# Optimization experiments

Measured on AMD Instinct MI355X. Metric: run time of the kernel, lower is better.

## Reference

```python
import jax, jax.numpy as jnp
import numpy as np

NUM_HEADS = 12
DIM_HEAD = 64
HIDDEN = 768


def _get_rel_pos(size, rel_pos):
    # q_size == k_size: relative coords in [0, 2*size-2]
    idx = jnp.arange(size)[:, None] - jnp.arange(size)[None, :] + (size - 1)
    return rel_pos[idx]  # (size, size, dim_head)


def setup_inputs() -> dict:
    key = jax.random.key(0)
    ks = jax.random.split(key, 5)
    B, H, W, C = 4, 32, 32, HIDDEN
    x = jax.random.normal(ks[0], (B, H, W, C), dtype=jnp.float32)
    w_qkv = jax.random.normal(ks[1], (C, 3 * NUM_HEADS * DIM_HEAD), dtype=jnp.float32) * (C ** -0.5)
    w_out = jax.random.normal(ks[2], (NUM_HEADS * DIM_HEAD, C), dtype=jnp.float32) * ((NUM_HEADS * DIM_HEAD) ** -0.5)
    b_out = jnp.zeros((C,), dtype=jnp.float32)
    rel_pos_h = jax.random.normal(ks[3], (2 * H - 1, DIM_HEAD), dtype=jnp.float32) * 0.02
    rel_pos_w = jax.random.normal(ks[4], (2 * W - 1, DIM_HEAD), dtype=jnp.float32) * 0.02
    return {"x": x, "w_qkv": w_qkv, "w_out": w_out, "b_out": b_out,
            "rel_pos_h": rel_pos_h, "rel_pos_w": rel_pos_w}


def reference(x, w_qkv, w_out, b_out, rel_pos_h, rel_pos_w):
    B, H, W, C = x.shape
    N = H * W
    nh, dh = NUM_HEADS, DIM_HEAD
    # qkv projection: (B, N, 3*nh*dh) split as (qkv, head, dim)
    qkv = x.reshape(B, N, C) @ w_qkv
    qkv = qkv.reshape(B, N, 3, nh, dh).transpose(2, 0, 3, 1, 4)  # (3, B, nh, N, dh)
    q, k, v = qkv[0], qkv[1], qkv[2]
    scale = dh ** -0.5
    attn = jnp.einsum('bhnd,bhmd->bhnm', q, k) * scale  # (B, nh, N, N)
    # decomposed relative positional bias (heads folded into batch)
    Rh = _get_rel_pos(H, rel_pos_h)  # (H, H, dh)
    Rw = _get_rel_pos(W, rel_pos_w)  # (W, W, dh)
    r_q = q.reshape(B * nh, H, W, dh)
    rel_h = jnp.einsum('bhwc,hkc->bhwk', r_q, Rh)  # (B*nh, H, W, H)
    rel_w = jnp.einsum('bhwc,wkc->bhwk', r_q, Rw)  # (B*nh, H, W, W)
    attn = (attn.reshape(B * nh, H, W, H, W)
            + rel_h[:, :, :, :, None]
            + rel_w[:, :, :, None, :]).reshape(B, nh, N, N)
    attn = jax.nn.softmax(attn, axis=-1)
    out = jnp.einsum('bhnm,bhmd->bhnd', attn, v)  # (B, nh, N, dh)
    out = out.transpose(0, 2, 1, 3).reshape(B, N, nh * dh)
    return out @ w_out + b_out  # (B, N, hidden)
```

## Files before the change

### kernel.cpp

```cpp
#include <hip/hip_runtime.h>
#include <cstdint>

#define DEV __device__ __forceinline__

typedef __bf16  bf16x8 __attribute__((ext_vector_type(8)));
typedef short   s16x8  __attribute__((ext_vector_type(8)));
typedef float   f32x4  __attribute__((ext_vector_type(4)));

#define QSCALE 0.18033688011112042f
#define MOFF   17.312340490667560f

DEV unsigned short f2bf(float f){
  union { float f; unsigned u; } v; v.f = f;
  unsigned r = v.u + 0x7fffu + ((v.u >> 16) & 1u);
  return (unsigned short)(r >> 16);
}

DEV unsigned pk2(float lo, float hi){
  unsigned a = __builtin_bit_cast(unsigned, lo) + 0x8000u;
  unsigned b = __builtin_bit_cast(unsigned, hi) + 0x8000u;
  return __builtin_amdgcn_perm(b, a, 0x07060302);
}

DEV void gl2lds16(const void* g, void* l){
  __builtin_amdgcn_global_load_lds((__attribute__((address_space(1))) void*)(void*)(g),
                                   (__attribute__((address_space(3))) void*)(l), 16, 0, 0);
}

DEV f32x4 mfma16(bf16x8 a, bf16x8 b, f32x4 c){
  return __builtin_amdgcn_mfma_f32_16x16x32_bf16(a, b, c, 0, 0, 0);
}

__global__ __launch_bounds__(256) void prep_kernel(const float* __restrict__ x,
                                                   short* __restrict__ xb,
                                                   const float* __restrict__ rph,
                                                   const float* __restrict__ rpw,
                                                   short* __restrict__ rphb,
                                                   short* __restrict__ rpwb,
                                                   const float* __restrict__ w_qkv,
                                                   short* __restrict__ wqT,
                                                   const float* __restrict__ w_out,
                                                   short* __restrict__ woT){
  __shared__ float tb[32][33];
  int b = blockIdx.x;
  if (b < 1536){
    int i = b * 256 + threadIdx.x;
    const float4* in4 = (const float4*)x;
    float4 f0 = in4[i*2], f1 = in4[i*2+1];
    s16x8 o;
    o[0]=(short)f2bf(f0.x); o[1]=(short)f2bf(f0.y); o[2]=(short)f2bf(f0.z); o[3]=(short)f2bf(f0.w);
    o[4]=(short)f2bf(f1.x); o[5]=(short)f2bf(f1.y); o[6]=(short)f2bf(f1.z); o[7]=(short)f2bf(f1.w);
    *(s16x8*)(xb + i*8) = o;
  } else if (b == 1536){
    int t = threadIdx.x;
    for (int j = 0; j < 16; j++){
      int idx = t*16 + j;
      if (idx < 4032){
        rphb[idx] = (short)f2bf(rph[idx] * 8.f);
        rpwb[idx] = (short)f2bf(rpw[idx] * 8.f);
      } else if (idx < 4096){
        rpwb[idx] = 0;
      }
    }
  } else {
    const float* in; short* out; int R, C, bx, by;
    if (b < 3265){ int t = b - 1537; in = w_qkv; out = wqT; R = 768; C = 2304; bx = t % 72; by = t / 72; }
    else         { int t = b - 3265; in = w_out; out = woT; R = 768; C = 768;  bx = t % 24; by = t / 24; }
    int tx = threadIdx.x & 31, ty = threadIdx.x >> 5;
    int c0 = bx * 32, r0 = by * 32;
    for (int i = 0; i < 4; i++)
      tb[ty + i*8][tx] = in[(r0 + ty + i*8)*C + c0 + tx];
    __syncthreads();
    for (int i = 0; i < 4; i++)
      out[(c0 + ty + i*8)*R + r0 + tx] = (short)f2bf(tb[tx][ty + i*8]);
  }
}

__global__ __launch_bounds__(256) void qkv_gemm_kernel(const short* __restrict__ xb,
                                                       const short* __restrict__ wqT,
                                                       short* __restrict__ qb,
                                                       short* __restrict__ kb,
                                                       short* __restrict__ vtb){
  __shared__ __align__(16) short As[128*64];
  __shared__ __align__(16) short Bs[96*64];
  const int tid = threadIdx.x, lane = tid & 63, wv = tid >> 6;
  const int quad = lane >> 4, mi = lane & 15;
  const int flat = blockIdx.x + (blockIdx.y << 5);
  const int xcd = flat & 7, s = flat >> 3;
  const int bx = (xcd & 3)*8 + (s & 7);
  const int by = (xcd >> 2)*12 + (s >> 3);
  const int m0 = bx * 128, n0 = by * 96;
  const int wrow = wv >> 1, wcol = wv & 1;
  const int srow = lane >> 3, scs = lane & 7;
  const int sc = scs ^ (srow & 7);
  f32x4 acc[4][3] = {};
  for (int k0 = 0; k0 < 768; k0 += 64){
    __syncthreads();
    for (int i = 0; i < 4; i++){
      int rbase = i*32 + wv*8;
      int row = rbase + srow;
      gl2lds16(xb + (m0+row)*768 + k0 + sc*8, As + rbase*64 + lane*8);
    }
    for (int i = 0; i < 3; i++){
      int rbase = i*32 + wv*8;
      int row = rbase + srow;
      gl2lds16(wqT + (n0+row)*768 + k0 + sc*8, Bs + rbase*64 + lane*8);
    }
    __syncthreads();
    bf16x8 a[2][4], b[2][3];
#pragma unroll
    for (int kk = 0; kk < 2; kk++){
      int ccs = ((quad + kk*4) ^ (mi & 7)) * 8;
      for (int mt = 0; mt < 4; mt++) a[kk][mt] = *(const bf16x8*)(As + (wrow*64 + mt*16 + mi)*64 + ccs);
      for (int nt = 0; nt < 3; nt++) b[kk][nt] = *(const bf16x8*)(Bs + (wcol*48 + nt*16 + mi)*64 + ccs);
    }
#pragma unroll
    for (int kk = 0; kk < 2; kk++)
      for (int mt = 0; mt < 4; mt++)
        for (int nt = 0; nt < 3; nt++)
          acc[mt][nt] = mfma16(a[kk][mt], b[kk][nt], acc[mt][nt]);
  }
  const int which = n0 / 768;
  if (which == 2){
    for (int nt = 0; nt < 3; nt++){
      int j = n0 + wcol*48 + nt*16 + mi;
      int rem = j % 768;
      int head = rem >> 6, d = rem & 63;
      for (int mt = 0; mt < 4; mt++)
        for (int r = 0; r < 4; r++){
          int m = m0 + wrow*64 + mt*16 + quad*4 + r;
          int bh = (m >> 10)*12 + head;
          vtb[((bh*64 + d) << 10) + (m & 1023)] = (short)f2bf(acc[mt][nt][r]);
        }
    }
  } else {
    const float qs = (which == 0) ? QSCALE : 1.0f;
    short* dst = (which == 0) ? qb : kb;
    for (int nt = 0; nt < 3; nt++){
      int j = n0 + wcol*48 + nt*16 + mi;
      int rem = j % 768;
      int head = rem >> 6, d = rem & 63;
      for (int mt = 0; mt < 4; mt++)
        for (int r = 0; r < 4; r++){
          int m = m0 + wrow*64 + mt*16 + quad*4 + r;
          int bh = (m >> 10)*12 + head;
          dst[((bh << 10) + (m & 1023))*64 + d] = (short)f2bf(acc[mt][nt][r] * qs);
        }
    }
  }
}

__global__ __launch_bounds__(256, 3) void flash_kernel(const short* __restrict__ qb,
                                                       const short* __restrict__ kb,
                                                       const short* __restrict__ vtb,
                                                       const short* __restrict__ rphb,
                                                       const short* __restrict__ rpwb,
                                                       short* __restrict__ ao){
  __shared__ __align__(16) char QE[16384];
  __shared__ __align__(16) short Kt[64*64];
  __shared__ __align__(16) short Vt[64*64];
  __shared__ __align__(16) short Pt[64*64];
  __shared__ __align__(16) float rHs[32*64];
  short* Qt = (short*)QE;
  float* Es = (float*)QE;
  const int tid = threadIdx.x, lane = tid & 63, wv = tid >> 6;
  const int quad = lane >> 4, mi = lane & 15;
  const int flat = blockIdx.x + (blockIdx.y << 4);
  const int nw = (flat & 7)*96 + (flat >> 3);
  const int bh = nw >> 4, n0 = (nw & 15) << 6;
  const int sw0 = (quad ^ (mi & 7)) * 8;
  const int sw1 = ((quad + 4) ^ (mi & 7)) * 8;
  const int qrow = wv*16 + mi;
  const int srow = lane >> 3;

  const short* kg = kb  + bh*1024*64;
  const short* vg = vtb + bh*64*1024;

  {
    const short* qg = qb + (bh*1024 + n0)*64;
    for (int i = 0; i < 2; i++){
      int slab = wv*2 + i, rbase = slab*8;
      int row = rbase + srow;
      int c = (lane & 7) ^ (row & 7);
      gl2lds16(qg + row*64 + c*8, Qt + rbase*64 + lane*8);
    }
  }
  __syncthreads();

  bf16x8 qf0 = *(const bf16x8*)(Qt + qrow*64 + sw0);
  bf16x8 qf1 = *(const bf16x8*)(Qt + qrow*64 + sw1);

  {
    int h = (n0 + wv*16) >> 5;
    const short* rp = rphb + (h + 31 - mi)*64;
#pragma unroll
    for (int khb = 0; khb < 2; khb++){
      const short* rk = rp - khb*1024;
      bf16x8 a0 = *(const bf16x8*)(rk + quad*8);
      bf16x8 a1 = *(const bf16x8*)(rk + 32 + quad*8);
      f32x4 c = {};
      c = mfma16(a0, qf0, c);
      c = mfma16(a1, qf1, c);
      for (int r = 0; r < 4; r++)
        rHs[(khb*16 + quad*4 + r)*64 + wv*16 + mi] = c[r] - MOFF;
    }
  }

  __syncthreads();

#pragma unroll
  for (int jt = 0; jt < 4; jt++){
    const short* rr = rpwb + (jt*16 + mi)*64;
    bf16x8 a0 = *(const bf16x8*)(rr + quad*8);
    bf16x8 a1 = *(const bf16x8*)(rr + 32 + quad*8);
    f32x4 c = {};
    c = mfma16(a0, qf0, c);
    c = mfma16(a1, qf1, c);
    for (int r = 0; r < 4; r++)
      Es[(jt*16 + quad*4 + r)*64 + qrow] = c[r];
  }
  float rw[2][4];
  {
    int w31 = (qrow & 31) + 31;
#pragma unroll
    for (int s = 0; s < 2; s++)
      for (int r = 0; r < 4; r++)
        rw[s][r] = Es[(w31 - (s*16 + quad*4 + r))*64 + qrow];
  }

  f32x4 O[4] = {};
  float l_ = 0.f;

  for (int step = 0; step < 16; step++){
    {
      const short* kt = kg + step*64*64;
      for (int i = 0; i < 2; i++){
        int slab = wv*2 + i, rbase = slab*8;
        int row = rbase + srow;
        int c = (lane & 7) ^ (row & 7);
        gl2lds16(kt + row*64 + c*8, Kt + rbase*64 + lane*8);
        gl2lds16(vg + row*1024 + step*64 + c*8, Vt + rbase*64 + lane*8);
      }
    }
    __syncthreads();

    f32x4 S[4];
#pragma unroll
    for (int nt = 0; nt < 4; nt++){
      bf16x8 kf0 = *(const bf16x8*)(Kt + (nt*16 + mi)*64 + sw0);
      bf16x8 kf1 = *(const bf16x8*)(Kt + (nt*16 + mi)*64 + sw1);
      f32x4 c = {};
      c = mfma16(kf0, qf0, c);
      c = mfma16(kf1, qf1, c);
      S[nt] = c;
    }
    float kh0 = rHs[(2*step)*64 + qrow];
    float kh1 = rHs[(2*step + 1)*64 + qrow];
#pragma unroll
    for (int nt = 0; nt < 4; nt++){
      float kh = (nt & 2) ? kh1 : kh0;
      for (int r = 0; r < 4; r++){
        float p = __builtin_amdgcn_exp2f(S[nt][r] + kh + rw[nt & 1][r]);
        S[nt][r] = p;
        l_ += p;
      }
    }
#pragma unroll
    for (int nt = 0; nt < 4; nt++){
      unsigned u0 = pk2(S[nt][0], S[nt][1]);
      unsigned u1 = pk2(S[nt][2], S[nt][3]);
      int chunk = (2*nt + (quad >> 1)) ^ (mi & 7);
      uint2 uu; uu.x = u0; uu.y = u1;
      *(uint2*)(Pt + qrow*64 + chunk*8 + (quad & 1)*4) = uu;
    }
    bf16x8 p0 = *(const bf16x8*)(Pt + qrow*64 + sw0);
    bf16x8 p1 = *(const bf16x8*)(Pt + qrow*64 + sw1);
#pragma unroll
    for (int t = 0; t < 4; t++){
      bf16x8 v0 = *(const bf16x8*)(Vt + (t*16 + mi)*64 + sw0);
      bf16x8 v1 = *(const bf16x8*)(Vt + (t*16 + mi)*64 + sw1);
      O[t] = mfma16(p0, v0, O[t]);
      O[t] = mfma16(p1, v1, O[t]);
    }
    __syncthreads();
  }

  l_ += __shfl_xor(l_, 16, 64);
  l_ += __shfl_xor(l_, 32, 64);
  float inv[4];
#pragma unroll
  for (int r = 0; r < 4; r++) inv[r] = 1.f / __shfl(l_, quad*4 + r, 64);
  int b_ = bh / 12, head = bh % 12;
#pragma unroll
  for (int t = 0; t < 4; t++)
    for (int r = 0; r < 4; r++){
      int n = n0 + wv*16 + quad*4 + r;
      ao[(b_*1024 + n)*768 + head*64 + t*16 + mi] = (short)f2bf(O[t][r] * inv[r]);
    }
}

__global__ __launch_bounds__(256) void proj_kernel(const short* __restrict__ ao,
                                                   const short* __restrict__ woT,
                                                   const float* __restrict__ bias,
                                                   float* __restrict__ out){
  __shared__ __align__(16) short As[64*64];
  __shared__ __align__(16) short Bs[96*64];
  const int tid = threadIdx.x, lane = tid & 63, wv = tid >> 6;
  const int quad = lane >> 4, mi = lane & 15;
  const int m0 = blockIdx.x * 64, n0 = blockIdx.y * 96;
  const int wrow = wv >> 1, wcol = wv & 1;
  const int srow = lane >> 3, sc = (lane & 7) ^ (srow & 7);
  f32x4 acc[2][3] = {};
  for (int k0 = 0; k0 < 768; k0 += 64){
    __syncthreads();
    for (int i = 0; i < 2; i++){
      int rbase = i*32 + wv*8, row = rbase + srow;
      gl2lds16(ao + (m0+row)*768 + k0 + sc*8, As + rbase*64 + lane*8);
    }
    for (int i = 0; i < 3; i++){
      int rbase = i*32 + wv*8, row = rbase + srow;
      gl2lds16(woT + (n0+row)*768 + k0 + sc*8, Bs + rbase*64 + lane*8);
    }
    __syncthreads();
    bf16x8 a[2][2], b[2][3];
#pragma unroll
    for (int kk = 0; kk < 2; kk++){
      int ccs = ((quad + kk*4) ^ (mi & 7)) * 8;
      for (int mt = 0; mt < 2; mt++) a[kk][mt] = *(const bf16x8*)(As + (wrow*32 + mt*16 + mi)*64 + ccs);
      for (int nt = 0; nt < 3; nt++) b[kk][nt] = *(const bf16x8*)(Bs + (wcol*48 + nt*16 + mi)*64 + ccs);
    }
#pragma unroll
    for (int kk = 0; kk < 2; kk++)
      for (int mt = 0; mt < 2; mt++)
        for (int nt = 0; nt < 3; nt++)
          acc[mt][nt] = mfma16(a[kk][mt], b[kk][nt], acc[mt][nt]);
  }
  for (int nt = 0; nt < 3; nt++){
    int j = n0 + wcol*48 + nt*16 + mi;
    float bj = bias[j];
    for (int mt = 0; mt < 2; mt++)
      for (int r = 0; r < 4; r++){
        int m = m0 + wrow*32 + mt*16 + quad*4 + r;
        out[m*768 + j] = acc[mt][nt][r] + bj;
      }
  }
}

extern "C" void kernel_launch(void* const* d_in, const int* in_sizes, int n_in,
                              void* d_out, int out_size, void* d_ws, size_t ws_size,
                              hipStream_t stream){
  const float* x     = (const float*)d_in[0];
  const float* w_qkv = (const float*)d_in[1];
  const float* w_out = (const float*)d_in[2];
  const float* b_out = (const float*)d_in[3];
  const float* rph   = (const float*)d_in[4];
  const float* rpw   = (const float*)d_in[5];
  float* out = (float*)d_out;
  char* ws = (char*)d_ws;
  short* xb    = (short*)(ws + 0);
  short* wqT   = (short*)(ws + 6291456);
  short* woT   = (short*)(ws + 9830400);
  short* qb    = (short*)(ws + 11010048);
  short* kb    = (short*)(ws + 17301504);
  short* vtb   = (short*)(ws + 29884416);
  short* rphb  = (short*)(ws + 48758784);
  short* rpwb  = (short*)(ws + 48775168);
  short* ao    = xb;

  prep_kernel<<<3841, 256, 0, stream>>>(x, xb, rph, rpw, rphb, rpwb, w_qkv, wqT, w_out, woT);
  qkv_gemm_kernel<<<dim3(32, 24), 256, 0, stream>>>(xb, wqT, qb, kb, vtb);
  flash_kernel<<<dim3(16, 48), 256, 0, stream>>>(qb, kb, vtb, rphb, rpwb, ao);
  proj_kernel<<<dim3(64, 8), 256, 0, stream>>>(ao, woT, b_out, out);
}
```

Before: 153.1 us.

## Double-buffer K/V tiles in flash kernel, reusing the Q/E scratch as second buffer

Restructures the attention main loop into a two-stage ping-pong. The next K/V tile is issued as async global-to-LDS copies while the current tile is computed, and the Q/Es shared region is reused as the second buffer so LDS size does not grow. The goal is to hide global load latency behind the MFMA and exp work and to drop one barrier per step. The risk is correctness around buffer reuse: Pt is written each step while only one barrier separates the stages, and the gl2lds copies must complete before the barrier.

```diff
diff --git a/kernel.cpp b/kernel.cpp
--- a/kernel.cpp
+++ b/kernel.cpp
@@ -157,12 +157,14 @@
                                                        const short* __restrict__ rpwb,
                                                        short* __restrict__ ao){
   __shared__ __align__(16) char QE[16384];
-  __shared__ __align__(16) short Kt[64*64];
-  __shared__ __align__(16) short Vt[64*64];
+  __shared__ __align__(16) short Kt0[64*64];
+  __shared__ __align__(16) short Vt0[64*64];
   __shared__ __align__(16) short Pt[64*64];
   __shared__ __align__(16) float rHs[32*64];
-  short* Qt = (short*)QE;
-  float* Es = (float*)QE;
+  short* Qt  = (short*)QE;
+  float* Es  = (float*)QE;
+  short* Kt1 = (short*)QE;
+  short* Vt1 = (short*)(QE + 8192);
   const int tid = threadIdx.x, lane = tid & 63, wv = tid >> 6;
   const int quad = lane >> 4, mi = lane & 15;
   const int flat = blockIdx.x + (blockIdx.y << 4);
@@ -176,14 +178,28 @@
   const short* kg = kb  + bh*1024*64;
   const short* vg = vtb + bh*64*1024;
 
+#define STAGE(Kd, Vd, stp) do{                                             \
+    const short* kt_ = kg + (stp)*4096;                                    \
+    _Pragma("unroll")                                                      \
+    for (int i_ = 0; i_ < 2; i_++){                                        \
+      int slab_ = wv*2 + i_, rbase_ = slab_*8;                             \
+      int row_ = rbase_ + srow;                                            \
+      int c_ = (lane & 7) ^ (row_ & 7);                                    \
+      gl2lds16(kt_ + row_*64 + c_*8, (Kd) + rbase_*64 + lane*8);           \
+      gl2lds16(vg + row_*1024 + (stp)*64 + c_*8, (Vd) + rbase_*64 + lane*8);\
+    }                                                                      \
+  }while(0)
+
   {
     const short* qg = qb + (bh*1024 + n0)*64;
+#pragma unroll
     for (int i = 0; i < 2; i++){
       int slab = wv*2 + i, rbase = slab*8;
       int row = rbase + srow;
       int c = (lane & 7) ^ (row & 7);
       gl2lds16(qg + row*64 + c*8, Qt + rbase*64 + lane*8);
     }
+    STAGE(Kt0, Vt0, 0);
   }
   __syncthreads();
 
@@ -228,62 +244,63 @@
         rw[s][r] = Es[(w31 - (s*16 + quad*4 + r))*64 + qrow];
   }
 
+  __syncthreads();
+
   f32x4 O[4] = {};
   float l_ = 0.f;
 
-  for (int step = 0; step < 16; step++){
-    {
-      const short* kt = kg + step*64*64;
-      for (int i = 0; i < 2; i++){
-        int slab = wv*2 + i, rbase = slab*8;
-        int row = rbase + srow;
-        int c = (lane & 7) ^ (row & 7);
-        gl2lds16(kt + row*64 + c*8, Kt + rbase*64 + lane*8);
-        gl2lds16(vg + row*1024 + step*64 + c*8, Vt + rbase*64 + lane*8);
-      }
-    }
-    __syncthreads();
-
-    f32x4 S[4];
-#pragma unroll
-    for (int nt = 0; nt < 4; nt++){
-      bf16x8 kf0 = *(const bf16x8*)(Kt + (nt*16 + mi)*64 + sw0);
-      bf16x8 kf1 = *(const bf16x8*)(Kt + (nt*16 + mi)*64 + sw1);
-      f32x4 c = {};
-      c = mfma16(kf0, qf0, c);
-      c = mfma16(kf1, qf1, c);
-      S[nt] = c;
-    }
-    float kh0 = rHs[(2*step)*64 + qrow];
-    float kh1 = rHs[(2*step + 1)*64 + qrow];
-#pragma unroll
-    for (int nt = 0; nt < 4; nt++){
-      float kh = (nt & 2) ? kh1 : kh0;
-      for (int r = 0; r < 4; r++){
-        float p = __builtin_amdgcn_exp2f(S[nt][r] + kh + rw[nt & 1][r]);
-        S[nt][r] = p;
-        l_ += p;
-      }
-    }
-#pragma unroll
-    for (int nt = 0; nt < 4; nt++){
-      unsigned u0 = pk2(S[nt][0], S[nt][1]);
-      unsigned u1 = pk2(S[nt][2], S[nt][3]);
-      int chunk = (2*nt + (quad >> 1)) ^ (mi & 7);
-      uint2 uu; uu.x = u0; uu.y = u1;
-      *(uint2*)(Pt + qrow*64 + chunk*8 + (quad & 1)*4) = uu;
-    }
-    bf16x8 p0 = *(const bf16x8*)(Pt + qrow*64 + sw0);
-    bf16x8 p1 = *(const bf16x8*)(Pt + qrow*64 + sw1);
-#pragma unroll
-    for (int t = 0; t < 4; t++){
-      bf16x8 v0 = *(const bf16x8*)(Vt + (t*16 + mi)*64 + sw0);
-      bf16x8 v1 = *(const bf16x8*)(Vt + (t*16 + mi)*64 + sw1);
-      O[t] = mfma16(p0, v0, O[t]);
-      O[t] = mfma16(p1, v1, O[t]);
-    }
-    __syncthreads();
-  }
+#define COMPUTE(Kb_, Vb_, stp) do{                                          \
+    f32x4 S_[4];                                                            \
+    _Pragma("unroll")                                                       \
+    for (int nt = 0; nt < 4; nt++){                                         \
+      bf16x8 kf0 = *(const bf16x8*)((Kb_) + (nt*16 + mi)*64 + sw0);         \
+      bf16x8 kf1 = *(const bf16x8*)((Kb_) + (nt*16 + mi)*64 + sw1);         \
+      f32x4 c_ = {};                                                        \
+      c_ = mfma16(kf0, qf0, c_);                                            \
+      c_ = mfma16(kf1, qf1, c_);                                            \
+      S_[nt] = c_;                                                          \
+    }                                                                       \
+    float kh0_ = rHs[(2*(stp))*64 + qrow];                                  \
+    float kh1_ = rHs[(2*(stp) + 1)*64 + qrow];                              \
+    _Pragma("unroll")                                                       \
+    for (int nt = 0; nt < 4; nt++){                                         \
+      float kh_ = (nt & 2) ? kh1_ : kh0_;                                   \
+      for (int r = 0; r < 4; r++){                                          \
+        float p_ = __builtin_amdgcn_exp2f(S_[nt][r] + kh_ + rw[nt & 1][r]); \
+        S_[nt][r] = p_;                                                     \
+        l_ += p_;                                                           \
+      }                                                                     \
+    }                                                                       \
+    _Pragma("unroll")                                                       \
+    for (int nt = 0; nt < 4; nt++){                                         \
+      unsigned u0_ = pk2(S_[nt][0], S_[nt][1]);                             \
+      unsigned u1_ = pk2(S_[nt][2], S_[nt][3]);                             \
+      int chunk_ = (2*nt + (quad >> 1)) ^ (mi & 7);                         \
+      uint2 uu_; uu_.x = u0_; uu_.y = u1_;                                  \
+      *(uint2*)(Pt + qrow*64 + chunk_*8 + (quad & 1)*4) = uu_;              \
+    }                                                                       \
+    bf16x8 p0_ = *(const bf16x8*)(Pt + qrow*64 + sw0);                      \
+    bf16x8 p1_ = *(const bf16x8*)(Pt + qrow*64 + sw1);                      \
+    _Pragma("unroll")                                                       \
+    for (int t = 0; t < 4; t++){                                            \
+      bf16x8 v0_ = *(const bf16x8*)((Vb_) + (t*16 + mi)*64 + sw0);          \
+      bf16x8 v1_ = *(const bf16x8*)((Vb_) + (t*16 + mi)*64 + sw1);          \
+      O[t] = mfma16(p0_, v0_, O[t]);                                        \
+      O[t] = mfma16(p1_, v1_, O[t]);                                        \
+    }                                                                       \
+  }while(0)
+
+#pragma unroll 1
+  for (int s2 = 0; s2 < 8; s2++){
+    STAGE(Kt1, Vt1, 2*s2 + 1);
+    COMPUTE(Kt0, Vt0, 2*s2);
+    __syncthreads();
+    if (s2 < 7) STAGE(Kt0, Vt0, 2*s2 + 2);
+    COMPUTE(Kt1, Vt1, 2*s2 + 1);
+    if (s2 < 7) __syncthreads();
+  }
+#undef STAGE
+#undef COMPUTE
 
   l_ += __shfl_xor(l_, 16, 64);
   l_ += __shfl_xor(l_, 32, 64);
```

New measurement: 151.0 us. No clear change (-1.4%).

## Shrink flash blocks to 32 rows and read K/V directly from global memory

Applied to the files above, without the earlier changes.

The flash attention kernel now uses 128-thread blocks covering 32 query rows (one image row) instead of 256 threads and 64 rows, doubling the grid. K and V tiles are no longer staged in shared memory; each wave loads its MFMA fragments straight from global memory, which removes the per-step __syncthreads barriers. Q fragments are also loaded directly, and the shared arrays for the relative-position tables use a padded stride of 33. The trade-off is that K/V reuse across waves now relies on cache rather than LDS, and the global loads are less coalesced.

```diff
diff --git a/kernel.cpp b/kernel.cpp
--- a/kernel.cpp
+++ b/kernel.cpp
@@ -91,8 +91,8 @@
   const int by = (xcd >> 2)*12 + (s >> 3);
   const int m0 = bx * 128, n0 = by * 96;
   const int wrow = wv >> 1, wcol = wv & 1;
-  const int srow = lane >> 3, scs = lane & 7;
-  const int sc = scs ^ (srow & 7);
+  const int srow = lane >> 3;
+  const int sc = (lane & 7) ^ (srow & 7);
   f32x4 acc[4][3] = {};
   for (int k0 = 0; k0 < 768; k0 += 64){
     __syncthreads();
@@ -150,49 +150,50 @@
   }
 }
 
-__global__ __launch_bounds__(256, 3) void flash_kernel(const short* __restrict__ qb,
+__global__ __launch_bounds__(128, 3) void flash_kernel(const short* __restrict__ qb,
                                                        const short* __restrict__ kb,
                                                        const short* __restrict__ vtb,
                                                        const short* __restrict__ rphb,
                                                        const short* __restrict__ rpwb,
                                                        short* __restrict__ ao){
-  __shared__ __align__(16) char QE[16384];
-  __shared__ __align__(16) short Kt[64*64];
-  __shared__ __align__(16) short Vt[64*64];
-  __shared__ __align__(16) short Pt[64*64];
-  __shared__ __align__(16) float rHs[32*64];
-  short* Qt = (short*)QE;
-  float* Es = (float*)QE;
+  __shared__ float Es[64*33];
+  __shared__ float rHs[32*33];
+  __shared__ __align__(16) short Pt[32*64];
   const int tid = threadIdx.x, lane = tid & 63, wv = tid >> 6;
   const int quad = lane >> 4, mi = lane & 15;
-  const int flat = blockIdx.x + (blockIdx.y << 4);
-  const int nw = (flat & 7)*96 + (flat >> 3);
-  const int bh = nw >> 4, n0 = (nw & 15) << 6;
+  const int flat = blockIdx.x + (blockIdx.y << 5);
+  const int nw = (flat & 7)*192 + (flat >> 3);
+  const int bh = nw >> 5, n0 = (nw & 31) << 5;
+  const int qrowL = wv*16 + mi;
   const int sw0 = (quad ^ (mi & 7)) * 8;
   const int sw1 = ((quad + 4) ^ (mi & 7)) * 8;
-  const int qrow = wv*16 + mi;
-  const int srow = lane >> 3;
-
-  const short* kg = kb  + bh*1024*64;
-  const short* vg = vtb + bh*64*1024;
+
+  const short* kg = kb  + bh*65536;
+  const short* vg = vtb + bh*65536;
+
+  const short* qr = qb + ((bh << 10) + n0 + qrowL)*64;
+  bf16x8 qf0 = *(const bf16x8*)(qr + quad*8);
+  bf16x8 qf1 = *(const bf16x8*)(qr + 32 + quad*8);
+
+#pragma unroll
+  for (int jt = 0; jt < 4; jt++){
+    const short* rr = rpwb + (jt*16 + mi)*64;
+    bf16x8 a0 = *(const bf16x8*)(rr + quad*8);
+    bf16x8 a1 = *(const bf16x8*)(rr + 32 + quad*8);
+    f32x4 c = {};
+    c = mfma16(a0, qf0, c);
+    c = mfma16(a1, qf1, c);
+    for (int r = 0; r < 4; r++)
+      Es[(jt*16 + quad*4 + r)*33 + qrowL] = c[r];
+  }
+  float rw[2][4];
+#pragma unroll
+  for (int s = 0; s < 2; s++)
+    for (int r = 0; r < 4; r++)
+      rw[s][r] = Es[(qrowL + 31 - (s*16 + quad*4 + r))*33 + qrowL];
 
   {
-    const short* qg = qb + (bh*1024 + n0)*64;
-    for (int i = 0; i < 2; i++){
-      int slab = wv*2 + i, rbase = slab*8;
-      int row = rbase + srow;
-      int c = (lane & 7) ^ (row & 7);
-      gl2lds16(qg + row*64 + c*8, Qt + rbase*64 + lane*8);
-    }
-  }
-  __syncthreads();
-
-  bf16x8 qf0 = *(const bf16x8*)(Qt + qrow*64 + sw0);
-  bf16x8 qf1 = *(const bf16x8*)(Qt + qrow*64 + sw1);
-
-  {
-    int h = (n0 + wv*16) >> 5;
-    const short* rp = rphb + (h + 31 - mi)*64;
+    const short* rp = rphb + ((nw & 31) + 31 - mi)*64;
 #pragma unroll
     for (int khb = 0; khb < 2; khb++){
       const short* rk = rp - khb*1024;
@@ -202,60 +203,29 @@
       c = mfma16(a0, qf0, c);
       c = mfma16(a1, qf1, c);
       for (int r = 0; r < 4; r++)
-        rHs[(khb*16 + quad*4 + r)*64 + wv*16 + mi] = c[r] - MOFF;
-    }
-  }
-
-  __syncthreads();
-
-#pragma unroll
-  for (int jt = 0; jt < 4; jt++){
-    const short* rr = rpwb + (jt*16 + mi)*64;
-    bf16x8 a0 = *(const bf16x8*)(rr + quad*8);
-    bf16x8 a1 = *(const bf16x8*)(rr + 32 + quad*8);
-    f32x4 c = {};
-    c = mfma16(a0, qf0, c);
-    c = mfma16(a1, qf1, c);
-    for (int r = 0; r < 4; r++)
-      Es[(jt*16 + quad*4 + r)*64 + qrow] = c[r];
-  }
-  float rw[2][4];
-  {
-    int w31 = (qrow & 31) + 31;
-#pragma unroll
-    for (int s = 0; s < 2; s++)
-      for (int r = 0; r < 4; r++)
-        rw[s][r] = Es[(w31 - (s*16 + quad*4 + r))*64 + qrow];
+        rHs[(khb*16 + quad*4 + r)*33 + qrowL] = c[r] - MOFF;
+    }
   }
 
   f32x4 O[4] = {};
   float l_ = 0.f;
 
+#pragma unroll 1
   for (int step = 0; step < 16; step++){
-    {
-      const short* kt = kg + step*64*64;
-      for (int i = 0; i < 2; i++){
-        int slab = wv*2 + i, rbase = slab*8;
-        int row = rbase + srow;
-        int c = (lane & 7) ^ (row & 7);
-        gl2lds16(kt + row*64 + c*8, Kt + rbase*64 + lane*8);
-        gl2lds16(vg + row*1024 + step*64 + c*8, Vt + rbase*64 + lane*8);
-      }
-    }
-    __syncthreads();
-
+    const short* kt = kg + step*4096;
     f32x4 S[4];
 #pragma unroll
     for (int nt = 0; nt < 4; nt++){
-      bf16x8 kf0 = *(const bf16x8*)(Kt + (nt*16 + mi)*64 + sw0);
-      bf16x8 kf1 = *(const bf16x8*)(Kt + (nt*16 + mi)*64 + sw1);
+      const short* krow = kt + (nt*16 + mi)*64;
+      bf16x8 kf0 = *(const bf16x8*)(krow + quad*8);
+      bf16x8 kf1 = *(const bf16x8*)(krow + 32 + quad*8);
       f32x4 c = {};
       c = mfma16(kf0, qf0, c);
       c = mfma16(kf1, qf1, c);
       S[nt] = c;
     }
-    float kh0 = rHs[(2*step)*64 + qrow];
-    float kh1 = rHs[(2*step + 1)*64 + qrow];
+    float kh0 = rHs[(2*step)*33 + qrowL];
+    float kh1 = rHs[(2*step + 1)*33 + qrowL];
 #pragma unroll
     for (int nt = 0; nt < 4; nt++){
       float kh = (nt & 2) ? kh1 : kh0;
@@ -271,18 +241,18 @@
       unsigned u1 = pk2(S[nt][2], S[nt][3]);
       int chunk = (2*nt + (quad >> 1)) ^ (mi & 7);
       uint2 uu; uu.x = u0; uu.y = u1;
-      *(uint2*)(Pt + qrow*64 + chunk*8 + (quad & 1)*4) = uu;
-    }
-    bf16x8 p0 = *(const bf16x8*)(Pt + qrow*64 + sw0);
-    bf16x8 p1 = *(const bf16x8*)(Pt + qrow*64 + sw1);
+      *(uint2*)(Pt + qrowL*64 + chunk*8 + (quad & 1)*4) = uu;
+    }
+    bf16x8 p0 = *(const bf16x8*)(Pt + qrowL*64 + sw0);
+    bf16x8 p1 = *(const bf16x8*)(Pt + qrowL*64 + sw1);
 #pragma unroll
     for (int t = 0; t < 4; t++){
-      bf16x8 v0 = *(const bf16x8*)(Vt + (t*16 + mi)*64 + sw0);
-      bf16x8 v1 = *(const bf16x8*)(Vt + (t*16 + mi)*64 + sw1);
+      const short* vrow = vg + (t*16 + mi)*1024 + step*64;
+      bf16x8 v0 = *(const bf16x8*)(vrow + quad*8);
+      bf16x8 v1 = *(const bf16x8*)(vrow + 32 + quad*8);
       O[t] = mfma16(p0, v0, O[t]);
       O[t] = mfma16(p1, v1, O[t]);
     }
-    __syncthreads();
   }
 
   l_ += __shfl_xor(l_, 16, 64);
@@ -369,6 +339,6 @@
 
   prep_kernel<<<3841, 256, 0, stream>>>(x, xb, rph, rpw, rphb, rpwb, w_qkv, wqT, w_out, woT);
   qkv_gemm_kernel<<<dim3(32, 24), 256, 0, stream>>>(xb, wqT, qb, kb, vtb);
-  flash_kernel<<<dim3(16, 48), 256, 0, stream>>>(qb, kb, vtb, rphb, rpwb, ao);
+  flash_kernel<<<dim3(32, 48), 128, 0, stream>>>(qb, kb, vtb, rphb, rpwb, ao);
   proj_kernel<<<dim3(64, 8), 256, 0, stream>>>(ao, woT, b_out, out);
 }
```

Measured after the change: 214.0 us. +39.8%, slower.
